# Kernel optimization log

Hardware: AMD Instinct MI355X
Metric: run time of the kernel (lower is better)

## Reference

```python
import jax, jax.numpy as jnp
import numpy as np

D_MODEL = 128
N_HEADS = 8
D_K = D_MODEL // N_HEADS
N_NODES = 50000
N_EDGES = 800000


def setup_inputs() -> dict:
    key = jax.random.key(0)
    ks = jax.random.split(key, 8)
    X = jax.random.normal(ks[0], (N_NODES, D_MODEL), dtype=jnp.float32)
    nbr_src = jax.random.randint(ks[1], (N_EDGES,), 0, N_NODES, dtype=jnp.int32)
    nbr_dst = jax.random.randint(ks[2], (N_EDGES,), 0, N_NODES, dtype=jnp.int32)
    s = 1.0 / np.sqrt(D_MODEL)
    W_qkv = jax.random.normal(ks[3], (3 * D_MODEL, D_MODEL), dtype=jnp.float32) * s
    w_bias = jax.random.normal(ks[4], (N_HEADS, D_MODEL), dtype=jnp.float32) * s
    W_gate = jax.random.normal(ks[5], (D_MODEL, D_MODEL), dtype=jnp.float32) * s
    b_gate = jax.random.normal(ks[6], (D_MODEL,), dtype=jnp.float32) * s
    W_o = jax.random.normal(ks[7], (D_MODEL, D_MODEL), dtype=jnp.float32) * s
    return {"X": X, "W_qkv": W_qkv, "w_bias": w_bias, "W_gate": W_gate,
            "b_gate": b_gate, "W_o": W_o, "nbr_src": nbr_src,
            "nbr_dst": nbr_dst, "num_cells": N_NODES}


def segment_softmax(scores, seg, num_segments):
    # scores: [E, H], seg: [E] -> softmax over edges sharing the same seg id
    mx = jax.ops.segment_max(scores, seg, num_segments=num_segments)  # [N, H]
    mx = jnp.where(jnp.isfinite(mx), mx, -1e9)
    exp_s = jnp.exp(scores - mx[seg])
    sm = jax.ops.segment_sum(exp_s, seg, num_segments=num_segments)  # [N, H]
    return exp_s / (sm[seg] + 1e-12)


def reference(X, W_qkv, w_bias, W_gate, b_gate, W_o, nbr_src, nbr_dst, num_cells):
    H, dk = N_HEADS, D_K
    scale = 1.0 / np.sqrt(dk)
    qkv = (X @ W_qkv.T).reshape(-1, 3, H, dk)      # [N, 3, H, dk]
    Q, K, V = qkv[:, 0], qkv[:, 1], qkv[:, 2]
    gate = jax.nn.sigmoid(X @ W_gate.T + b_gate).reshape(-1, H, dk)
    bias = X @ w_bias.T                             # [N, H]
    scores = jnp.einsum('ehd,ehd->eh', Q[nbr_src], K[nbr_dst]) * scale + bias[nbr_src]
    attn = segment_softmax(scores, nbr_src, num_cells)          # [E, H]
    out = jax.ops.segment_sum(attn[:, :, None] * V[nbr_dst], nbr_src,
                              num_segments=num_cells)           # [N, H, dk]
    return (gate * out).reshape(-1, D_MODEL) @ W_o.T
```

## Files before the change

kernel.cpp:

```cpp
#include <hip/hip_runtime.h>
#include <hip/hip_fp16.h>

#define DM 128
#define NHEADS 8
#define MAXDEG 64
#define SROW 136

typedef _Float16 half8 __attribute__((ext_vector_type(8)));
typedef _Float16 half2v __attribute__((ext_vector_type(2)));
typedef float floatx4 __attribute__((ext_vector_type(4)));

union H8 { half8 v; half2v h2[4]; };

__device__ __forceinline__ void prefetch_B(
    int tid, int c, const float* __restrict__ Wqkv,
    const float* __restrict__ Wgate, const float* __restrict__ wbias,
    float4 pf[4][2]) {
#pragma unroll
  for (int i = 0; i < 4; i++) {
    int u = tid + i * 256;
    int r = u >> 4;
    int cc = (u & 15) * 8;
    int grow = c * 64 + r;
    const float* src = nullptr;
    if (grow < 384)      src = Wqkv + (size_t)grow * 128 + cc;
    else if (grow < 512) src = Wgate + (size_t)(grow - 384) * 128 + cc;
    else if (grow < 520) src = wbias + (size_t)(grow - 512) * 128 + cc;
    if (src) {
      pf[i][0] = ((const float4*)src)[0];
      pf[i][1] = ((const float4*)src)[1];
    } else {
      pf[i][0] = make_float4(0.f, 0.f, 0.f, 0.f);
      pf[i][1] = make_float4(0.f, 0.f, 0.f, 0.f);
    }
  }
}

__global__ __launch_bounds__(256) void proj_csr(
    const float* __restrict__ X, const float* __restrict__ Wqkv,
    const float* __restrict__ Wgate, const float* __restrict__ wbias,
    const float* __restrict__ b_gate,
    const int* __restrict__ nsrc, const int* __restrict__ ndst,
    int* __restrict__ cnt, unsigned short* __restrict__ csr_dst,
    _Float16* __restrict__ Q, _Float16* __restrict__ KV,
    _Float16* __restrict__ gate, float* __restrict__ bias,
    int M, int E, int P) {
  __shared__ _Float16 As[128 * SROW];
  __shared__ _Float16 Bs[64 * SROW];
  int tid = threadIdx.x;
  int bid = blockIdx.x;

  if (bid >= P) {
    int ebase = (bid - P) * 8192;
    for (int g = 0; g < 4; g++) {
      int s[8], d[8];
#pragma unroll
      for (int j = 0; j < 8; j++) {
        int e = ebase + (g * 8 + j) * 256 + tid;
        s[j] = (e < E) ? __builtin_nontemporal_load(nsrc + e) : -1;
        d[j] = (e < E) ? __builtin_nontemporal_load(ndst + e) : 0;
      }
#pragma unroll
      for (int j = 0; j < 8; j++) {
        if (s[j] >= 0) {
          int p = atomicAdd(&cnt[s[j]], 1);
          if (p < MAXDEG) csr_dst[(size_t)s[j] * MAXDEG + p] = (unsigned short)d[j];
        }
      }
    }
    return;
  }

  int m0 = bid * 128;

  float4 pf[4][2];
  prefetch_B(tid, 0, Wqkv, Wgate, wbias, pf);

#pragma unroll
  for (int i = 0; i < 4; i++) {
    int u = tid + i * 256;
    int r = u >> 3;
    int cc = (u & 7) * 16;
    int gr = m0 + r;
    float4 f0, f1, f2, f3;
    if (gr < M) {
      const float4* src = (const float4*)(X + (size_t)gr * 128 + cc);
      f0 = src[0]; f1 = src[1]; f2 = src[2]; f3 = src[3];
    } else {
      f0 = f1 = f2 = f3 = make_float4(0.f, 0.f, 0.f, 0.f);
    }
    half8 h0 = {(_Float16)f0.x, (_Float16)f0.y, (_Float16)f0.z, (_Float16)f0.w,
                (_Float16)f1.x, (_Float16)f1.y, (_Float16)f1.z, (_Float16)f1.w};
    half8 h1 = {(_Float16)f2.x, (_Float16)f2.y, (_Float16)f2.z, (_Float16)f2.w,
                (_Float16)f3.x, (_Float16)f3.y, (_Float16)f3.z, (_Float16)f3.w};
    *(half8*)(As + r * SROW + cc) = h0;
    *(half8*)(As + r * SROW + cc + 8) = h1;
  }

  int wid = tid >> 6, lane = tid & 63;
  int quad = lane >> 4, l16 = lane & 15;
  int mw = wid * 32;

  for (int c = 0; c < 9; c++) {
    __syncthreads();
#pragma unroll
    for (int i = 0; i < 4; i++) {
      int u = tid + i * 256;
      int r = u >> 4;
      int cc = (u & 15) * 8;
      half8 h = {(_Float16)pf[i][0].x, (_Float16)pf[i][0].y,
                 (_Float16)pf[i][0].z, (_Float16)pf[i][0].w,
                 (_Float16)pf[i][1].x, (_Float16)pf[i][1].y,
                 (_Float16)pf[i][1].z, (_Float16)pf[i][1].w};
      *(half8*)(Bs + r * SROW + cc) = h;
    }
    if (c < 8) prefetch_B(tid, c + 1, Wqkv, Wgate, wbias, pf);
    __syncthreads();

    floatx4 acc[2][4] = {};
#pragma unroll
    for (int kc = 0; kc < 4; kc++) {
      int ko = kc * 32 + quad * 8;
      half8 a0 = *(const half8*)(As + (mw + l16) * SROW + ko);
      half8 a1 = *(const half8*)(As + (mw + 16 + l16) * SROW + ko);
      half8 b[4];
#pragma unroll
      for (int ni = 0; ni < 4; ni++)
        b[ni] = *(const half8*)(Bs + (ni * 16 + l16) * SROW + ko);
#pragma unroll
      for (int ni = 0; ni < 4; ni++) {
        acc[0][ni] = __builtin_amdgcn_mfma_f32_16x16x32_f16(a0, b[ni], acc[0][ni], 0, 0, 0);
        acc[1][ni] = __builtin_amdgcn_mfma_f32_16x16x32_f16(a1, b[ni], acc[1][ni], 0, 0, 0);
      }
    }

    if (c == 8) {
      if (l16 < 8) {
#pragma unroll
        for (int mi = 0; mi < 2; mi++)
#pragma unroll
          for (int r = 0; r < 4; r++) {
            int row = m0 + mw + mi * 16 + quad * 4 + r;
            if (row < M) bias[(size_t)row * 8 + l16] = acc[mi][0][r];
          }
      }
    } else {
      int reg = c >> 1;
#pragma unroll
      for (int mi = 0; mi < 2; mi++) {
#pragma unroll
        for (int ni = 0; ni < 4; ni++) {
          int colL = (c & 1) * 64 + ni * 16 + l16;
#pragma unroll
          for (int r = 0; r < 4; r++) {
            int row = m0 + mw + mi * 16 + quad * 4 + r;
            if (row >= M) continue;
            float v = acc[mi][ni][r];
            if (reg == 0)      Q[(size_t)row * 128 + colL] = (_Float16)v;
            else if (reg == 1) KV[(size_t)row * 256 + colL] = (_Float16)v;
            else if (reg == 2) KV[(size_t)row * 256 + 128 + colL] = (_Float16)v;
            else gate[(size_t)row * 128 + colL] =
                   (_Float16)(1.0f / (1.0f + __expf(-(v + b_gate[colL]))));
          }
        }
      }
    }
  }
}

__global__ __launch_bounds__(256) void final_gemm_mfma(
    const _Float16* __restrict__ A, const float* __restrict__ Wo,
    float* __restrict__ C, int M) {
  __shared__ _Float16 As[128 * SROW];
  __shared__ _Float16 Bs[64 * SROW];
  int tid = threadIdx.x;
  int m0 = blockIdx.x * 128, n0 = blockIdx.y * 64;
#pragma unroll
  for (int i = 0; i < 8; i++) {
    int u = tid + i * 256;
    int r = u >> 4;
    int cc = (u & 15) * 8;
    int gr = m0 + r;
    int4 val = make_int4(0, 0, 0, 0);
    if (gr < M) val = *(const int4*)(A + (size_t)gr * 128 + cc);
    *(int4*)(As + r * SROW + cc) = val;
  }
#pragma unroll
  for (int i = 0; i < 4; i++) {
    int u = tid + i * 256;
    int r = u >> 4;
    int cc = (u & 15) * 8;
    const float* src = Wo + (size_t)(n0 + r) * 128 + cc;
    float4 f0 = ((const float4*)src)[0];
    float4 f1 = ((const float4*)src)[1];
    half8 h = {(_Float16)f0.x, (_Float16)f0.y, (_Float16)f0.z, (_Float16)f0.w,
               (_Float16)f1.x, (_Float16)f1.y, (_Float16)f1.z, (_Float16)f1.w};
    *(half8*)(Bs + r * SROW + cc) = h;
  }
  __syncthreads();

  int wid = tid >> 6, lane = tid & 63;
  int quad = lane >> 4, l16 = lane & 15;
  int mw = (wid >> 1) * 64;
  int nw = (wid & 1) * 32;

  floatx4 acc[4][2] = {};
#pragma unroll
  for (int kc = 0; kc < 4; kc++) {
    int ko = kc * 32 + quad * 8;
    half8 a[4], b[2];
#pragma unroll
    for (int mi = 0; mi < 4; mi++)
      a[mi] = *(const half8*)(As + (mw + mi * 16 + l16) * SROW + ko);
#pragma unroll
    for (int ni = 0; ni < 2; ni++)
      b[ni] = *(const half8*)(Bs + (nw + ni * 16 + l16) * SROW + ko);
#pragma unroll
    for (int mi = 0; mi < 4; mi++)
#pragma unroll
      for (int ni = 0; ni < 2; ni++)
        acc[mi][ni] = __builtin_amdgcn_mfma_f32_16x16x32_f16(a[mi], b[ni], acc[mi][ni], 0, 0, 0);
  }
#pragma unroll
  for (int mi = 0; mi < 4; mi++) {
#pragma unroll
    for (int ni = 0; ni < 2; ni++) {
      int col = n0 + nw + ni * 16 + l16;
#pragma unroll
      for (int r = 0; r < 4; r++) {
        int row = m0 + mw + mi * 16 + quad * 4 + r;
        if (row >= M) continue;
        C[(size_t)row * 128 + col] = acc[mi][ni][r];
      }
    }
  }
}

__global__ __launch_bounds__(256) void attn_fused(
    const int* __restrict__ cnt, const unsigned short* __restrict__ csr_dst,
    const _Float16* __restrict__ Q, const _Float16* __restrict__ KV,
    const float* __restrict__ bias, const _Float16* __restrict__ gate,
    _Float16* __restrict__ gated, int N) {
  int wave = threadIdx.x >> 6, lane = threadIdx.x & 63;
  int n = blockIdx.x * 4 + wave;
  if (n >= N) return;
  int deg = __builtin_nontemporal_load(cnt + n);
  if (deg > MAXDEG) deg = MAXDEG;
  int qtr = lane >> 4, l16 = lane & 15;
  int ch0 = l16 * 8;

  int dstv = (int)__builtin_nontemporal_load(csr_dst + (size_t)n * MAXDEG + lane);

  H8 qu; qu.v = __builtin_nontemporal_load((const half8*)(Q + (size_t)n * DM + ch0));
  float bias_h = __builtin_nontemporal_load(bias + (size_t)n * NHEADS + (l16 >> 1));

  float acc[8] = {};
  float den = 0.f;
  int iters = (deg + 3) >> 2;

  H8 kb[4], vb[4];
  bool bb[4];
#pragma unroll
  for (int j = 0; j < 4; j++) {
    bb[j] = false;
    kb[j].v = half8{}; vb[j].v = half8{};
    if (j < iters) {
      int e = j * 4 + qtr;
      bb[j] = e < deg;
      int d = __shfl(dstv, e);
      d = bb[j] ? d : 0;
      const _Float16* kvp = KV + (size_t)d * 256 + ch0;
      kb[j].v = *(const half8*)kvp;
      vb[j].v = *(const half8*)(kvp + 128);
    }
  }

  for (int base = 0; base < iters; base += 4) {
#pragma unroll
    for (int j = 0; j < 4; j++) {
      float p = 0.f;
#pragma unroll
      for (int t = 0; t < 4; t++)
        p = __builtin_amdgcn_fdot2(qu.h2[t], kb[j].h2[t], p, false);
      p += __shfl_xor(p, 1);
      float w = __expf(p * 0.25f + bias_h);
      if (!bb[j]) w = 0.f;
      den += w;
#pragma unroll
      for (int t = 0; t < 8; t++) acc[t] = fmaf(w, (float)vb[j].v[t], acc[t]);
      int idx = base + 4 + j;
      bb[j] = false;
      if (idx < iters) {
        int e = idx * 4 + qtr;
        bb[j] = e < deg;
        int d = __shfl(dstv, e);
        d = bb[j] ? d : 0;
        const _Float16* kvp = KV + (size_t)d * 256 + ch0;
        kb[j].v = *(const half8*)kvp;
        vb[j].v = *(const half8*)(kvp + 128);
      }
    }
  }

#pragma unroll
  for (int j = 0; j < 8; j++) acc[j] += __shfl_xor(acc[j], 16);
#pragma unroll
  for (int j = 0; j < 8; j++) acc[j] += __shfl_xor(acc[j], 32);
  den += __shfl_xor(den, 16);
  den += __shfl_xor(den, 32);

  if (qtr == 0) {
    float inv = 1.0f / (den + 1e-12f);
    half8 gv = __builtin_nontemporal_load((const half8*)(gate + (size_t)n * DM + ch0));
    half8 o;
#pragma unroll
    for (int j = 0; j < 8; j++) o[j] = (_Float16)(acc[j] * inv * (float)gv[j]);
    __builtin_nontemporal_store(o, (half8*)(gated + (size_t)n * DM + ch0));
  }
}

extern "C" void kernel_launch(void* const* d_in, const int* in_sizes, int n_in,
                              void* d_out, int out_size, void* d_ws, size_t ws_size,
                              hipStream_t stream) {
  const float* X     = (const float*)d_in[0];
  const float* Wqkv  = (const float*)d_in[1];
  const float* wbias = (const float*)d_in[2];
  const float* Wgate = (const float*)d_in[3];
  const float* bgate = (const float*)d_in[4];
  const float* Wo    = (const float*)d_in[5];
  const int*   nsrc  = (const int*)d_in[6];
  const int*   ndst  = (const int*)d_in[7];
  int N = in_sizes[0] / 128;
  int E = in_sizes[6];
  float* out = (float*)d_out;

  char* p = (char*)d_ws;
  _Float16* Q16     = (_Float16*)p; p += (size_t)N * 128 * sizeof(_Float16);
  _Float16* KV16    = (_Float16*)p; p += (size_t)N * 256 * sizeof(_Float16);
  _Float16* gate16  = (_Float16*)p; p += (size_t)N * 128 * sizeof(_Float16);
  _Float16* gated16 = (_Float16*)p; p += (size_t)N * 128 * sizeof(_Float16);
  float* bias       = (float*)p;    p += (size_t)N * 8 * sizeof(float);
  int* cnt          = (int*)p;      p += (size_t)N * sizeof(int);
  unsigned short* csr_dst = (unsigned short*)p;
  p += (size_t)N * MAXDEG * sizeof(unsigned short);

  hipMemsetAsync(cnt, 0, (size_t)N * sizeof(int), stream);

  int P = (N + 127) / 128;
  int C = (E + 8191) / 8192;
  proj_csr<<<P + C, 256, 0, stream>>>(X, Wqkv, Wgate, wbias, bgate, nsrc, ndst,
                                      cnt, csr_dst, Q16, KV16, gate16, bias, N, E, P);

  attn_fused<<<(N + 3) / 4, 256, 0, stream>>>(cnt, csr_dst, Q16, KV16, bias,
                                              gate16, gated16, N);

  dim3 fg((N + 127) / 128, 2);
  final_gemm_mfma<<<fg, 256, 0, stream>>>(gated16, Wo, out, N);
}
```

Before: 230.8 us.

## Revert to int CSR, drop B-tile register prefetch and nontemporal hints

Changes the CSR neighbor list from 16-bit to 32-bit indices, which doubles its footprint and traffic. Removes the register double-buffering prefetch of weight tiles in the projection GEMM, so each chunk now loads its weights synchronously between barriers. Moves the b_gate bias loads into registers ahead of the loop, and switches several nontemporal loads and stores to plain ones. This looks like rolling back several earlier micro-optimizations together, trading latency hiding and bandwidth for simpler code and lower register pressure.

```diff
diff --git a/kernel.cpp b/kernel.cpp
--- a/kernel.cpp
+++ b/kernel.cpp
@@ -11,37 +11,13 @@
 typedef float floatx4 __attribute__((ext_vector_type(4)));
 
 union H8 { half8 v; half2v h2[4]; };
-
-__device__ __forceinline__ void prefetch_B(
-    int tid, int c, const float* __restrict__ Wqkv,
-    const float* __restrict__ Wgate, const float* __restrict__ wbias,
-    float4 pf[4][2]) {
-#pragma unroll
-  for (int i = 0; i < 4; i++) {
-    int u = tid + i * 256;
-    int r = u >> 4;
-    int cc = (u & 15) * 8;
-    int grow = c * 64 + r;
-    const float* src = nullptr;
-    if (grow < 384)      src = Wqkv + (size_t)grow * 128 + cc;
-    else if (grow < 512) src = Wgate + (size_t)(grow - 384) * 128 + cc;
-    else if (grow < 520) src = wbias + (size_t)(grow - 512) * 128 + cc;
-    if (src) {
-      pf[i][0] = ((const float4*)src)[0];
-      pf[i][1] = ((const float4*)src)[1];
-    } else {
-      pf[i][0] = make_float4(0.f, 0.f, 0.f, 0.f);
-      pf[i][1] = make_float4(0.f, 0.f, 0.f, 0.f);
-    }
-  }
-}
 
 __global__ __launch_bounds__(256) void proj_csr(
     const float* __restrict__ X, const float* __restrict__ Wqkv,
     const float* __restrict__ Wgate, const float* __restrict__ wbias,
     const float* __restrict__ b_gate,
     const int* __restrict__ nsrc, const int* __restrict__ ndst,
-    int* __restrict__ cnt, unsigned short* __restrict__ csr_dst,
+    int* __restrict__ cnt, int* __restrict__ csr_dst,
     _Float16* __restrict__ Q, _Float16* __restrict__ KV,
     _Float16* __restrict__ gate, float* __restrict__ bias,
     int M, int E, int P) {
@@ -57,14 +33,14 @@
 #pragma unroll
       for (int j = 0; j < 8; j++) {
         int e = ebase + (g * 8 + j) * 256 + tid;
-        s[j] = (e < E) ? __builtin_nontemporal_load(nsrc + e) : -1;
-        d[j] = (e < E) ? __builtin_nontemporal_load(ndst + e) : 0;
+        s[j] = (e < E) ? nsrc[e] : -1;
+        d[j] = (e < E) ? ndst[e] : 0;
       }
 #pragma unroll
       for (int j = 0; j < 8; j++) {
         if (s[j] >= 0) {
           int p = atomicAdd(&cnt[s[j]], 1);
-          if (p < MAXDEG) csr_dst[(size_t)s[j] * MAXDEG + p] = (unsigned short)d[j];
+          if (p < MAXDEG) csr_dst[(size_t)s[j] * MAXDEG + p] = d[j];
         }
       }
     }
@@ -72,9 +48,6 @@
   }
 
   int m0 = bid * 128;
-
-  float4 pf[4][2];
-  prefetch_B(tid, 0, Wqkv, Wgate, wbias, pf);
 
 #pragma unroll
   for (int i = 0; i < 4; i++) {
@@ -101,6 +74,13 @@
   int quad = lane >> 4, l16 = lane & 15;
   int mw = wid * 32;
 
+  float bg0[4], bg1[4];
+#pragma unroll
+  for (int ni = 0; ni < 4; ni++) {
+    bg0[ni] = b_gate[ni * 16 + l16];
+    bg1[ni] = b_gate[64 + ni * 16 + l16];
+  }
+
   for (int c = 0; c < 9; c++) {
     __syncthreads();
 #pragma unroll
@@ -108,13 +88,20 @@
       int u = tid + i * 256;
       int r = u >> 4;
       int cc = (u & 15) * 8;
-      half8 h = {(_Float16)pf[i][0].x, (_Float16)pf[i][0].y,
-                 (_Float16)pf[i][0].z, (_Float16)pf[i][0].w,
-                 (_Float16)pf[i][1].x, (_Float16)pf[i][1].y,
-                 (_Float16)pf[i][1].z, (_Float16)pf[i][1].w};
+      int grow = c * 64 + r;
+      const float* src = nullptr;
+      if (grow < 384)      src = Wqkv + (size_t)grow * 128 + cc;
+      else if (grow < 512) src = Wgate + (size_t)(grow - 384) * 128 + cc;
+      else if (grow < 520) src = wbias + (size_t)(grow - 512) * 128 + cc;
+      half8 h = {};
+      if (src) {
+        float4 f0 = ((const float4*)src)[0];
+        float4 f1 = ((const float4*)src)[1];
+        h = half8{(_Float16)f0.x, (_Float16)f0.y, (_Float16)f0.z, (_Float16)f0.w,
+                  (_Float16)f1.x, (_Float16)f1.y, (_Float16)f1.z, (_Float16)f1.w};
+      }
       *(half8*)(Bs + r * SROW + cc) = h;
     }
-    if (c < 8) prefetch_B(tid, c + 1, Wqkv, Wgate, wbias, pf);
     __syncthreads();
 
     floatx4 acc[2][4] = {};
@@ -151,6 +138,7 @@
 #pragma unroll
         for (int ni = 0; ni < 4; ni++) {
           int colL = (c & 1) * 64 + ni * 16 + l16;
+          float bgv = (c & 1) ? bg1[ni] : bg0[ni];
 #pragma unroll
           for (int r = 0; r < 4; r++) {
             int row = m0 + mw + mi * 16 + quad * 4 + r;
@@ -160,7 +148,7 @@
             else if (reg == 1) KV[(size_t)row * 256 + colL] = (_Float16)v;
             else if (reg == 2) KV[(size_t)row * 256 + 128 + colL] = (_Float16)v;
             else gate[(size_t)row * 128 + colL] =
-                   (_Float16)(1.0f / (1.0f + __expf(-(v + b_gate[colL]))));
+                   (_Float16)(1.0f / (1.0f + __expf(-(v + bgv))));
           }
         }
       }
@@ -237,7 +225,7 @@
 }
 
 __global__ __launch_bounds__(256) void attn_fused(
-    const int* __restrict__ cnt, const unsigned short* __restrict__ csr_dst,
+    const int* __restrict__ cnt, const int* __restrict__ csr_dst,
     const _Float16* __restrict__ Q, const _Float16* __restrict__ KV,
     const float* __restrict__ bias, const _Float16* __restrict__ gate,
     _Float16* __restrict__ gated, int N) {
@@ -249,7 +237,7 @@
   int qtr = lane >> 4, l16 = lane & 15;
   int ch0 = l16 * 8;
 
-  int dstv = (int)__builtin_nontemporal_load(csr_dst + (size_t)n * MAXDEG + lane);
+  int dstv = __builtin_nontemporal_load(csr_dst + (size_t)n * MAXDEG + lane);
 
   H8 qu; qu.v = __builtin_nontemporal_load((const half8*)(Q + (size_t)n * DM + ch0));
   float bias_h = __builtin_nontemporal_load(bias + (size_t)n * NHEADS + (l16 >> 1));
@@ -315,7 +303,7 @@
     half8 o;
 #pragma unroll
     for (int j = 0; j < 8; j++) o[j] = (_Float16)(acc[j] * inv * (float)gv[j]);
-    __builtin_nontemporal_store(o, (half8*)(gated + (size_t)n * DM + ch0));
+    *(half8*)(gated + (size_t)n * DM + ch0) = o;
   }
 }
 
@@ -341,8 +329,7 @@
   _Float16* gated16 = (_Float16*)p; p += (size_t)N * 128 * sizeof(_Float16);
   float* bias       = (float*)p;    p += (size_t)N * 8 * sizeof(float);
   int* cnt          = (int*)p;      p += (size_t)N * sizeof(int);
-  unsigned short* csr_dst = (unsigned short*)p;
-  p += (size_t)N * MAXDEG * sizeof(unsigned short);
+  int* csr_dst      = (int*)p;      p += (size_t)N * MAXDEG * sizeof(int);
 
   hipMemsetAsync(cnt, 0, (size_t)N * sizeof(int), stream);
 
```

Result: faster. 217.2 us (-5.9%).
